# Kernel optimization log

Measured on AMD Instinct MI355X. Metric: run time of the kernel, lower is better.

The kernel has to match this reference:

```python
import jax, jax.numpy as jnp
import numpy as np

B, S, D, H, L = 32, 512, 512, 8, 6
NQ, FF, V, C = 8, 2048, 32000, 10
DK = D // H
EPS = 1e-5


def _layernorm(x, g, b):
    mu = jnp.mean(x, axis=-1, keepdims=True)
    var = jnp.mean(jnp.square(x - mu), axis=-1, keepdims=True)
    return (x - mu) * jax.lax.rsqrt(var + EPS) * g + b


def _pos_encoding(seq_len, dim):
    pos = jnp.arange(seq_len, dtype=jnp.float32)[:, None]
    div = jnp.exp(jnp.arange(0, dim, 2, dtype=jnp.float32) * (-jnp.log(10000.0) / dim))
    pe = jnp.zeros((seq_len, dim), dtype=jnp.float32)
    pe = pe.at[:, 0::2].set(jnp.sin(pos * div))
    pe = pe.at[:, 1::2].set(jnp.cos(pos * div))
    return pe


def setup_inputs() -> dict:
    key = jax.random.key(0)
    ks = jax.random.split(key, 16)
    sd = 0.02
    return {
        "x": jax.random.randint(ks[0], (B, S), 0, V),
        "emb": jax.random.normal(ks[1], (V, D), jnp.float32) * sd,
        "ln1_g": jnp.ones((L, D), jnp.float32),
        "ln1_b": jnp.zeros((L, D), jnp.float32),
        "ln2_g": jnp.ones((L, D), jnp.float32),
        "ln2_b": jnp.zeros((L, D), jnp.float32),
        "attn_w": jax.random.normal(ks[2], (L, D, D), jnp.float32) * sd,
        "attn_b": jnp.zeros((L, D), jnp.float32),
        "theta": jax.random.normal(ks[3], (L, NQ), jnp.float32),
        "ffn_w1": jax.random.normal(ks[4], (L, NQ, FF), jnp.float32) * sd,
        "ffn_b1": jnp.zeros((L, FF), jnp.float32),
        "ffn_w2": jax.random.normal(ks[5], (L, FF, D), jnp.float32) * sd,
        "ffn_b2": jnp.zeros((L, D), jnp.float32),
        "clf_w": jax.random.normal(ks[6], (D, C), jnp.float32) * sd,
        "clf_b": jnp.zeros((C,), jnp.float32),
    }


def reference(x, emb, ln1_g, ln1_b, ln2_g, ln2_b, attn_w, attn_b, theta,
              ffn_w1, ffn_b1, ffn_w2, ffn_b2, clf_w, clf_b):
    h = emb[x] + _pos_encoding(S, D)[None]  # [B,S,D]
    scale = 1.0 / jnp.sqrt(jnp.float32(DK))
    for l in range(L):
        # --- MultiHeadAttentionQuantum: q=k=v=reshape(x), no projections ---
        q = h.reshape(B, S, H, DK)
        scores = jnp.einsum('bihd,bjhd->bhij', q, q) * scale
        p = jax.nn.softmax(scores, axis=-1)
        attn = jnp.einsum('bhij,bjhd->bihd', p, q).reshape(B, S, D)
        attn = attn @ attn_w[l] + attn_b[l]
        h = _layernorm(h + attn, ln1_g[l], ln1_b[l])
        # --- FeedForwardQuantum: per-wire RX-encode -> RY(theta) -> <Z> = cos(x)cos(theta) ---
        qout = jnp.cos(h[..., :NQ]) * jnp.cos(theta[l])  # [B,S,NQ]
        f = jax.nn.relu(qout @ ffn_w1[l] + ffn_b1[l]) @ ffn_w2[l] + ffn_b2[l]
        h = _layernorm(h + f, ln2_g[l], ln2_b[l])
    pooled = jnp.mean(h, axis=1)  # [B,D]
    return pooled @ clf_w + clf_b  # [B,C]
```

## Files before the change

### kernel.cpp

```cpp
#include <hip/hip_runtime.h>
#include <hip/hip_bf16.h>
#include <math.h>

#define BB 32
#define SS 512
#define DD 512
#define HH 8
#define DK 64
#define LL 6
#define NQ 8
#define FF 2048
#define CC 10

typedef unsigned int uint;
typedef unsigned short ushort_t;
using bf16x8 = __attribute__((ext_vector_type(8))) short;
using f32x4  = __attribute__((ext_vector_type(4))) float;

#define MFMA(a, b, c) __builtin_amdgcn_mfma_f32_16x16x32_bf16((a), (b), (c), 0, 0, 0)

union U8 { ushort_t u[8]; bf16x8 v; };

__device__ inline ushort_t f2bf(float x) {
    uint u = __float_as_uint(x);
    u += 0x7FFFu + ((u >> 16) & 1u);
    return (ushort_t)(u >> 16);
}
__device__ inline void tsplit(float v, ushort_t& hi, ushort_t& lo) {
    uint u = __float_as_uint(v);
    hi = (ushort_t)(u >> 16);
    lo = f2bf(v - __uint_as_float(u & 0xFFFF0000u));
}
__device__ inline void tsplit_fast(float v, ushort_t& hi, ushort_t& lo) {
    uint u = __float_as_uint(v);
    hi = (ushort_t)(u >> 16);
    float res = v - __uint_as_float(u & 0xFFFF0000u);
    lo = (ushort_t)(__float_as_uint(res) >> 16);
}
__device__ inline uint packsplit(float v) {
    uint u = __float_as_uint(v) & 0xFFFF0000u;
    uint ru = __float_as_uint(v - __uint_as_float(u));
    ru += 0x7FFFu + ((ru >> 16) & 1u);
    return u | (ru >> 16);
}
__device__ inline float unpackf(uint u) {
    return __uint_as_float(u & 0xFFFF0000u) + __uint_as_float(u << 16);
}

__global__ __launch_bounds__(256) void embed_pe(const int* __restrict__ x,
                                                const float* __restrict__ emb,
                                                uint* __restrict__ Hp) {
    int idx = blockIdx.x * 256 + threadIdx.x;
    if (idx >= BB * SS * DD) return;
    int d = idx & (DD - 1);
    int s = (idx >> 9) & (SS - 1);
    int tok = x[idx >> 9];
    int i2 = d >> 1;
    float freq = expf((float)(2 * i2) * (-9.210340371976184f / (float)DD));
    float ang = (float)s * freq;
    float pe = (d & 1) ? cosf(ang) : sinf(ang);
    Hp[idx] = packsplit(emb[(size_t)tok * DD + d] + pe);
}

__global__ __launch_bounds__(256) void transpose_split_w(const float* __restrict__ in,
                                                         ushort_t* __restrict__ outh,
                                                         ushort_t* __restrict__ outl,
                                                         int K, int N) {
    __shared__ ushort_t th[64][68], tl[64][68];
    int nb = N >> 6;
    int k0 = ((int)blockIdx.x / nb) << 6;
    int n0 = ((int)blockIdx.x % nb) << 6;
    int t = threadIdx.x;
    int r = t >> 2, cb = (t & 3) << 4;
#pragma unroll
    for (int c = 0; c < 4; c++) {
        float4 v = *reinterpret_cast<const float4*>(&in[(size_t)(k0 + r) * N + n0 + cb + 4 * c]);
        float vv[4] = {v.x, v.y, v.z, v.w};
#pragma unroll
        for (int e = 0; e < 4; e++) {
            ushort_t hb, lb; tsplit(vv[e], hb, lb);
            th[r][cb + 4 * c + e] = hb;
            tl[r][cb + 4 * c + e] = lb;
        }
    }
    __syncthreads();
    int n = t >> 2, kb = (t & 3) << 4;
#pragma unroll
    for (int c = 0; c < 4; c++) {
        ushort4 oh, ol;
        oh.x = th[kb + 4 * c + 0][n]; ol.x = tl[kb + 4 * c + 0][n];
        oh.y = th[kb + 4 * c + 1][n]; ol.y = tl[kb + 4 * c + 1][n];
        oh.z = th[kb + 4 * c + 2][n]; ol.z = tl[kb + 4 * c + 2][n];
        oh.w = th[kb + 4 * c + 3][n]; ol.w = tl[kb + 4 * c + 3][n];
        *reinterpret_cast<ushort4*>(&outh[(size_t)(n0 + n) * K + k0 + kb + 4 * c]) = oh;
        *reinterpret_cast<ushort4*>(&outl[(size_t)(n0 + n) * K + k0 + kb + 4 * c]) = ol;
    }
}

__global__ __launch_bounds__(256) void prep_w1t(const float* __restrict__ W1all,
                                                ushort_t* __restrict__ outh,
                                                ushort_t* __restrict__ outl) {
    int l = blockIdx.y;
    int f = blockIdx.x * 256 + threadIdx.x;
    const float* W1 = W1all + (size_t)l * NQ * FF;
    U8 ph, pl;
#pragma unroll
    for (int n = 0; n < 8; n++) {
        ushort_t hb, lb; tsplit(W1[n * FF + f], hb, lb);
        ph.u[n] = hb; pl.u[n] = lb;
    }
    *reinterpret_cast<bf16x8*>(&outh[((size_t)l * FF + f) * 8]) = ph.v;
    *reinterpret_cast<bf16x8*>(&outl[((size_t)l * FF + f) * 8]) = pl.v;
}

__global__ __launch_bounds__(256, 2) void flash_attn_split(const uint* __restrict__ Hp,
                                                           ushort_t* __restrict__ outh,
                                                           ushort_t* __restrict__ outl) {
    __shared__ __align__(16) ushort_t Qh[64][72], Ql[64][72];
    __shared__ __align__(16) ushort_t Kh[64][72], Kl[64][72];
    __shared__ __align__(16) ushort_t Vh[64][72], Vl[64][72];
    __shared__ __align__(16) ushort_t Ph[64][72], Pl[64][72];

    int i0 = blockIdx.x * 64;
    int h0 = blockIdx.y * DK;
    int b  = blockIdx.z;
    const uint* baseH = Hp + (size_t)b * (SS * DD);

    int t = threadIdx.x;
    int w = t >> 6;
    int ln = t & 63;
    int l15 = ln & 15, lh = ln >> 4;

    {
        int r = t >> 2, cb = (t & 3) << 4;
        const uint* src = &baseH[(size_t)(i0 + r) * DD + h0 + cb];
#pragma unroll
        for (int g = 0; g < 2; g++) {
            U8 qh, ql;
#pragma unroll
            for (int c = 0; c < 2; c++) {
                uint4 pv = *reinterpret_cast<const uint4*>(src + g * 8 + c * 4);
                uint uu[4] = {pv.x, pv.y, pv.z, pv.w};
#pragma unroll
                for (int e = 0; e < 4; e++) {
                    qh.u[c * 4 + e] = (ushort_t)(uu[e] >> 16);
                    ql.u[c * 4 + e] = (ushort_t)(uu[e] & 0xFFFFu);
                }
            }
            *reinterpret_cast<bf16x8*>(&Qh[r][cb + g * 8]) = qh.v;
            *reinterpret_cast<bf16x8*>(&Ql[r][cb + g * 8]) = ql.v;
        }
    }

    float m_[4], l_[4], al[4];
    f32x4 acc[4];
    f32x4 z4 = {0.f, 0.f, 0.f, 0.f};
#pragma unroll
    for (int r = 0; r < 4; r++) { m_[r] = -1e30f; l_[r] = 0.f; acc[r] = z4; }

    for (int j0 = 0; j0 < SS; j0 += 64) {
        __syncthreads();
        {
            int r = t >> 2, cb = (t & 3) << 4;
            const uint* src = &baseH[(size_t)(j0 + r) * DD + h0 + cb];
#pragma unroll
            for (int g = 0; g < 2; g++) {
                U8 kh, kl;
#pragma unroll
                for (int c = 0; c < 2; c++) {
                    uint4 pv = *reinterpret_cast<const uint4*>(src + g * 8 + c * 4);
                    uint uu[4] = {pv.x, pv.y, pv.z, pv.w};
#pragma unroll
                    for (int e = 0; e < 4; e++) {
                        ushort_t hb = (ushort_t)(uu[e] >> 16);
                        ushort_t lb = (ushort_t)(uu[e] & 0xFFFFu);
                        kh.u[c * 4 + e] = hb;
                        kl.u[c * 4 + e] = lb;
                        int d = cb + g * 8 + c * 4 + e;
                        Vh[d][r] = hb;
                        Vl[d][r] = lb;
                    }
                }
                *reinterpret_cast<bf16x8*>(&Kh[r][cb + g * 8]) = kh.v;
                *reinterpret_cast<bf16x8*>(&Kl[r][cb + g * 8]) = kl.v;
            }
        }
        __syncthreads();

        f32x4 sc[4];
        bf16x8 aqh0 = *reinterpret_cast<const bf16x8*>(&Qh[w * 16 + l15][lh * 8]);
        bf16x8 aqh1 = *reinterpret_cast<const bf16x8*>(&Qh[w * 16 + l15][32 + lh * 8]);
        bf16x8 aql0 = *reinterpret_cast<const bf16x8*>(&Ql[w * 16 + l15][lh * 8]);
        bf16x8 aql1 = *reinterpret_cast<const bf16x8*>(&Ql[w * 16 + l15][32 + lh * 8]);
#pragma unroll
        for (int tt = 0; tt < 4; tt++) {
            bf16x8 bh0 = *reinterpret_cast<const bf16x8*>(&Kh[tt * 16 + l15][lh * 8]);
            bf16x8 bh1 = *reinterpret_cast<const bf16x8*>(&Kh[tt * 16 + l15][32 + lh * 8]);
            bf16x8 bl0 = *reinterpret_cast<const bf16x8*>(&Kl[tt * 16 + l15][lh * 8]);
            bf16x8 bl1 = *reinterpret_cast<const bf16x8*>(&Kl[tt * 16 + l15][32 + lh * 8]);
            f32x4 s = z4;
            s = MFMA(aqh0, bh0, s);
            s = MFMA(aqh1, bh1, s);
            s = MFMA(aqh0, bl0, s);
            s = MFMA(aqh1, bl1, s);
            s = MFMA(aql0, bh0, s);
            s = MFMA(aql1, bh1, s);
            sc[tt] = s * 0.125f;
        }

#pragma unroll
        for (int r = 0; r < 4; r++) {
            float mx = fmaxf(fmaxf(sc[0][r], sc[1][r]), fmaxf(sc[2][r], sc[3][r]));
            mx = fmaxf(mx, __shfl_xor(mx, 1));
            mx = fmaxf(mx, __shfl_xor(mx, 2));
            mx = fmaxf(mx, __shfl_xor(mx, 4));
            mx = fmaxf(mx, __shfl_xor(mx, 8));
            float nm = fmaxf(m_[r], mx);
            al[r] = __expf(m_[r] - nm);
            m_[r] = nm;
            float rs = 0.f;
#pragma unroll
            for (int tt = 0; tt < 4; tt++) {
                float p = __expf(sc[tt][r] - nm);
                sc[tt][r] = p;
                rs += p;
            }
            rs += __shfl_xor(rs, 1);
            rs += __shfl_xor(rs, 2);
            rs += __shfl_xor(rs, 4);
            rs += __shfl_xor(rs, 8);
            l_[r] = l_[r] * al[r] + rs;
        }
#pragma unroll
        for (int tt = 0; tt < 4; tt++)
#pragma unroll
            for (int r = 0; r < 4; r++) {
                ushort_t hb, lb; tsplit(sc[tt][r], hb, lb);
                Ph[w * 16 + lh * 4 + r][tt * 16 + l15] = hb;
                Pl[w * 16 + lh * 4 + r][tt * 16 + l15] = lb;
            }
#pragma unroll
        for (int td = 0; td < 4; td++) {
            acc[td][0] *= al[0];
            acc[td][1] *= al[1];
            acc[td][2] *= al[2];
            acc[td][3] *= al[3];
        }
        bf16x8 aph0 = *reinterpret_cast<const bf16x8*>(&Ph[w * 16 + l15][lh * 8]);
        bf16x8 aph1 = *reinterpret_cast<const bf16x8*>(&Ph[w * 16 + l15][32 + lh * 8]);
        bf16x8 apl0 = *reinterpret_cast<const bf16x8*>(&Pl[w * 16 + l15][lh * 8]);
        bf16x8 apl1 = *reinterpret_cast<const bf16x8*>(&Pl[w * 16 + l15][32 + lh * 8]);
#pragma unroll
        for (int td = 0; td < 4; td++) {
            bf16x8 bvh0 = *reinterpret_cast<const bf16x8*>(&Vh[td * 16 + l15][lh * 8]);
            bf16x8 bvh1 = *reinterpret_cast<const bf16x8*>(&Vh[td * 16 + l15][32 + lh * 8]);
            bf16x8 bvl0 = *reinterpret_cast<const bf16x8*>(&Vl[td * 16 + l15][lh * 8]);
            bf16x8 bvl1 = *reinterpret_cast<const bf16x8*>(&Vl[td * 16 + l15][32 + lh * 8]);
            acc[td] = MFMA(aph0, bvh0, acc[td]);
            acc[td] = MFMA(aph1, bvh1, acc[td]);
            acc[td] = MFMA(aph0, bvl0, acc[td]);
            acc[td] = MFMA(aph1, bvl1, acc[td]);
            acc[td] = MFMA(apl0, bvh0, acc[td]);
            acc[td] = MFMA(apl1, bvh1, acc[td]);
        }
    }

#pragma unroll
    for (int r = 0; r < 4; r++) {
        float inv = 1.f / l_[r];
        int row = i0 + w * 16 + lh * 4 + r;
#pragma unroll
        for (int td = 0; td < 4; td++) {
            float o = acc[td][r] * inv;
            ushort_t hb, lb; tsplit(o, hb, lb);
            size_t idx = (size_t)b * SS * DD + (size_t)row * DD + h0 + td * 16 + l15;
            outh[idx] = hb;
            outl[idx] = lb;
        }
    }
}

__global__ __launch_bounds__(256, 2) void gemm_split(const ushort_t* __restrict__ Ah,
                                                     const ushort_t* __restrict__ Al,
                                                     const ushort_t* __restrict__ Bth,
                                                     const ushort_t* __restrict__ Btl,
                                                     const float* __restrict__ bias,
                                                     float* __restrict__ C,
                                                     int M, int N, int K) {
    __shared__ __align__(16) ushort_t Abh[128][72], Abl[128][72];
    __shared__ __align__(16) ushort_t Bbh[128][72], Bbl[128][72];
    int nb = N >> 7;
    int m0 = ((int)blockIdx.x / nb) << 7;
    int n0 = ((int)blockIdx.x % nb) << 7;
    int t = threadIdx.x;
    int w = t >> 6, ln = t & 63, l15 = ln & 15, lh = ln >> 4;
    int wr = (w >> 1) * 64, wc = (w & 1) * 64;

    f32x4 z4 = {0.f, 0.f, 0.f, 0.f};
    f32x4 acc[4][4];
#pragma unroll
    for (int i = 0; i < 4; i++)
#pragma unroll
        for (int j = 0; j < 4; j++) acc[i][j] = z4;

    int arr = t >> 3, akk = (t & 7) * 8;

    for (int k0 = 0; k0 < K; k0 += 64) {
        __syncthreads();
#pragma unroll
        for (int r = 0; r < 4; r++) {
            int row = arr + r * 32;
            *reinterpret_cast<uint4*>(&Abh[row][akk]) =
                *reinterpret_cast<const uint4*>(&Ah[(size_t)(m0 + row) * K + k0 + akk]);
            *reinterpret_cast<uint4*>(&Abl[row][akk]) =
                *reinterpret_cast<const uint4*>(&Al[(size_t)(m0 + row) * K + k0 + akk]);
            *reinterpret_cast<uint4*>(&Bbh[row][akk]) =
                *reinterpret_cast<const uint4*>(&Bth[(size_t)(n0 + row) * K + k0 + akk]);
            *reinterpret_cast<uint4*>(&Bbl[row][akk]) =
                *reinterpret_cast<const uint4*>(&Btl[(size_t)(n0 + row) * K + k0 + akk]);
        }
        __syncthreads();
#pragma unroll
        for (int ks = 0; ks < 2; ks++) {
            bf16x8 ah[4], al_[4];
#pragma unroll
            for (int mt = 0; mt < 4; mt++) {
                ah[mt]  = *reinterpret_cast<const bf16x8*>(&Abh[wr + mt * 16 + l15][ks * 32 + lh * 8]);
                al_[mt] = *reinterpret_cast<const bf16x8*>(&Abl[wr + mt * 16 + l15][ks * 32 + lh * 8]);
            }
#pragma unroll
            for (int nt = 0; nt < 4; nt++) {
                bf16x8 bh = *reinterpret_cast<const bf16x8*>(&Bbh[wc + nt * 16 + l15][ks * 32 + lh * 8]);
                bf16x8 bl = *reinterpret_cast<const bf16x8*>(&Bbl[wc + nt * 16 + l15][ks * 32 + lh * 8]);
#pragma unroll
                for (int mt = 0; mt < 4; mt++) {
                    acc[mt][nt] = MFMA(ah[mt], bh, acc[mt][nt]);
                    acc[mt][nt] = MFMA(ah[mt], bl, acc[mt][nt]);
                    acc[mt][nt] = MFMA(al_[mt], bh, acc[mt][nt]);
                }
            }
        }
    }
#pragma unroll
    for (int nt = 0; nt < 4; nt++) {
        int col = n0 + wc + nt * 16 + l15;
        float bs = bias[col];
#pragma unroll
        for (int mt = 0; mt < 4; mt++)
#pragma unroll
            for (int r = 0; r < 4; r++)
                C[(size_t)(m0 + wr + mt * 16 + lh * 4 + r) * N + col] = acc[mt][nt][r] + bs;
    }
}

__global__ __launch_bounds__(256) void ln_residual(uint* __restrict__ Hp,
                                                   const float* __restrict__ add,
                                                   const float* __restrict__ g,
                                                   const float* __restrict__ bta) {
    int row = blockIdx.x * 4 + (threadIdx.x >> 6);
    int lane = threadIdx.x & 63;
    uint* hp = Hp + (size_t)row * DD;
    const float* ap = add + (size_t)row * DD;
    float v[8];
    float sum = 0.f;
#pragma unroll
    for (int i = 0; i < 8; i++) {
        int d = lane + i * 64;
        v[i] = unpackf(hp[d]) + ap[d];
        sum += v[i];
    }
#pragma unroll
    for (int off = 32; off > 0; off >>= 1) sum += __shfl_xor(sum, off);
    float mu = sum * (1.f / DD);
    float s2 = 0.f;
#pragma unroll
    for (int i = 0; i < 8; i++) {
        float d2 = v[i] - mu;
        s2 += d2 * d2;
    }
#pragma unroll
    for (int off = 32; off > 0; off >>= 1) s2 += __shfl_xor(s2, off);
    float inv = rsqrtf(s2 * (1.f / DD) + 1e-5f);
#pragma unroll
    for (int i = 0; i < 8; i++) {
        int d = lane + i * 64;
        hp[d] = packsplit((v[i] - mu) * inv * g[d] + bta[d]);
    }
}

__global__ __launch_bounds__(256, 2) void ffn_split(const uint* __restrict__ Hp,
                                                    const ushort_t* __restrict__ W1th,
                                                    const ushort_t* __restrict__ W1tl,
                                                    const float* __restrict__ b1,
                                                    const ushort_t* __restrict__ W2th,
                                                    const ushort_t* __restrict__ W2tl,
                                                    const float* __restrict__ b2,
                                                    const float* __restrict__ theta,
                                                    float* __restrict__ outp) {
    __shared__ __align__(16) ushort_t Abh[128][72], Abl[128][72];
    __shared__ __align__(16) ushort_t Bbh[128][72], Bbl[128][72];
    __shared__ __align__(16) ushort_t qsh[129][8], qsl[129][8];
    __shared__ float tcs[8];

    int t = threadIdx.x;
    int m0 = (int)(blockIdx.x >> 2) * 128;
    int n0 = (int)(blockIdx.x & 3) * 128;
    if (t < 8) {
        tcs[t] = cosf(theta[t]);
        qsh[128][t] = 0;
        qsl[128][t] = 0;
    }
    __syncthreads();
#pragma unroll
    for (int i = 0; i < 4; i++) {
        int idx = t + i * 256;
        int m = idx >> 3, n = idx & 7;
        float q = cosf(unpackf(Hp[(size_t)(m0 + m) * DD + n])) * tcs[n];
        ushort_t hb, lb; tsplit(q, hb, lb);
        qsh[m][n] = hb;
        qsl[m][n] = lb;
    }

    int w = t >> 6, ln = t & 63, l15 = ln & 15, lh = ln >> 4;
    int wr = (w >> 1) * 64, wc = (w & 1) * 64;
    bool lh0 = (lh == 0);
    f32x4 z4 = {0.f, 0.f, 0.f, 0.f};
    bf16x8 z8 = {0, 0, 0, 0, 0, 0, 0, 0};
    f32x4 acc[4][4];
#pragma unroll
    for (int i = 0; i < 4; i++)
#pragma unroll
        for (int j = 0; j < 4; j++) acc[i][j] = z4;

    int brr = t >> 3, bkk = (t & 7) * 8;

    for (int k0 = 0; k0 < FF; k0 += 64) {
        __syncthreads();
#pragma unroll
        for (int r = 0; r < 4; r++) {
            int row = brr + r * 32;
            *reinterpret_cast<uint4*>(&Bbh[row][bkk]) =
                *reinterpret_cast<const uint4*>(&W2th[(size_t)(n0 + row) * FF + k0 + bkk]);
            *reinterpret_cast<uint4*>(&Bbl[row][bkk]) =
                *reinterpret_cast<const uint4*>(&W2tl[(size_t)(n0 + row) * FF + k0 + bkk]);
        }
        bf16x8 wh[4], wl[4];
#pragma unroll
        for (int fq = 0; fq < 4; fq++) {
            bf16x8 h8 = *reinterpret_cast<const bf16x8*>(&W1th[(size_t)(k0 + fq * 16 + l15) * 8]);
            bf16x8 l8 = *reinterpret_cast<const bf16x8*>(&W1tl[(size_t)(k0 + fq * 16 + l15) * 8]);
            wh[fq] = lh0 ? h8 : z8;
            wl[fq] = lh0 ? l8 : z8;
        }
#pragma unroll
        for (int mqi = 0; mqi < 2; mqi++) {
            int m = (w * 2 + mqi) * 16 + l15;
            int mrow = lh0 ? m : 128;
            bf16x8 qh  = *reinterpret_cast<const bf16x8*>(&qsh[mrow][0]);
            bf16x8 ql_ = *reinterpret_cast<const bf16x8*>(&qsl[mrow][0]);
#pragma unroll
            for (int fq = 0; fq < 4; fq++) {
                f32x4 d = z4;
                d = MFMA(wh[fq], qh, d);
                d = MFMA(wh[fq], ql_, d);
                d = MFMA(wl[fq], qh, d);
                float4 b1v = *reinterpret_cast<const float4*>(&b1[k0 + fq * 16 + lh * 4]);
                float v0 = fmaxf(d[0] + b1v.x, 0.f);
                float v1 = fmaxf(d[1] + b1v.y, 0.f);
                float v2 = fmaxf(d[2] + b1v.z, 0.f);
                float v3 = fmaxf(d[3] + b1v.w, 0.f);
                ushort_t h0_, l0_, h1_, l1_, h2_, l2_, h3_, l3_;
                tsplit_fast(v0, h0_, l0_);
                tsplit_fast(v1, h1_, l1_);
                tsplit_fast(v2, h2_, l2_);
                tsplit_fast(v3, h3_, l3_);
                uint2 hu, lu;
                hu.x = (uint)h0_ | ((uint)h1_ << 16);
                hu.y = (uint)h2_ | ((uint)h3_ << 16);
                lu.x = (uint)l0_ | ((uint)l1_ << 16);
                lu.y = (uint)l2_ | ((uint)l3_ << 16);
                *reinterpret_cast<uint2*>(&Abh[m][fq * 16 + lh * 4]) = hu;
                *reinterpret_cast<uint2*>(&Abl[m][fq * 16 + lh * 4]) = lu;
            }
        }
        __syncthreads();
#pragma unroll
        for (int ks = 0; ks < 2; ks++) {
            bf16x8 ah[4], al_[4];
#pragma unroll
            for (int mt = 0; mt < 4; mt++) {
                ah[mt]  = *reinterpret_cast<const bf16x8*>(&Abh[wr + mt * 16 + l15][ks * 32 + lh * 8]);
                al_[mt] = *reinterpret_cast<const bf16x8*>(&Abl[wr + mt * 16 + l15][ks * 32 + lh * 8]);
            }
#pragma unroll
            for (int nt = 0; nt < 4; nt++) {
                bf16x8 bh = *reinterpret_cast<const bf16x8*>(&Bbh[wc + nt * 16 + l15][ks * 32 + lh * 8]);
                bf16x8 bl = *reinterpret_cast<const bf16x8*>(&Bbl[wc + nt * 16 + l15][ks * 32 + lh * 8]);
#pragma unroll
                for (int mt = 0; mt < 4; mt++) {
                    acc[mt][nt] = MFMA(ah[mt], bh, acc[mt][nt]);
                    acc[mt][nt] = MFMA(ah[mt], bl, acc[mt][nt]);
                    acc[mt][nt] = MFMA(al_[mt], bh, acc[mt][nt]);
                }
            }
        }
    }
#pragma unroll
    for (int nt = 0; nt < 4; nt++) {
        int col = n0 + wc + nt * 16 + l15;
        float bs = b2[col];
#pragma unroll
        for (int mt = 0; mt < 4; mt++)
#pragma unroll
            for (int r = 0; r < 4; r++)
                outp[(size_t)(m0 + wr + mt * 16 + lh * 4 + r) * DD + col] = acc[mt][nt][r] + bs;
    }
}

__global__ __launch_bounds__(256) void pool_mean(const uint* __restrict__ Hp,
                                                 float* __restrict__ pooled) {
    int idx = blockIdx.x * 256 + threadIdx.x;
    if (idx >= BB * DD) return;
    int b = idx >> 9, d = idx & 511;
    float s = 0.f;
    for (int j = 0; j < SS; j++) s += unpackf(Hp[((size_t)b * SS + j) * DD + d]);
    pooled[idx] = s * (1.f / SS);
}

__global__ __launch_bounds__(64) void classifier(const float* __restrict__ pooled,
                                                 const float* __restrict__ W,
                                                 const float* __restrict__ bias,
                                                 float* __restrict__ out) {
    int o = blockIdx.x;
    int b = o / CC, c = o % CC;
    int lane = threadIdx.x;
    float s = 0.f;
    for (int d = lane; d < DD; d += 64) s += pooled[b * DD + d] * W[d * CC + c];
#pragma unroll
    for (int off = 32; off > 0; off >>= 1) s += __shfl_xor(s, off);
    if (lane == 0) out[o] = s + bias[c];
}

extern "C" void kernel_launch(void* const* d_in, const int* in_sizes, int n_in,
                              void* d_out, int out_size, void* d_ws, size_t ws_size,
                              hipStream_t stream) {
    (void)in_sizes; (void)n_in; (void)out_size; (void)ws_size;
    const int*   x      = (const int*)d_in[0];
    const float* emb    = (const float*)d_in[1];
    const float* ln1_g  = (const float*)d_in[2];
    const float* ln1_b  = (const float*)d_in[3];
    const float* ln2_g  = (const float*)d_in[4];
    const float* ln2_b  = (const float*)d_in[5];
    const float* attn_w = (const float*)d_in[6];
    const float* attn_b = (const float*)d_in[7];
    const float* theta  = (const float*)d_in[8];
    const float* ffn_w1 = (const float*)d_in[9];
    const float* ffn_b1 = (const float*)d_in[10];
    const float* ffn_w2 = (const float*)d_in[11];
    const float* ffn_b2 = (const float*)d_in[12];
    const float* clf_w  = (const float*)d_in[13];
    const float* clf_b  = (const float*)d_in[14];
    float* out = (float*)d_out;

    char* ws = (char*)d_ws;
    uint*     Hp     = (uint*)(ws);
    float*    t2     = (float*)(ws + 33554432);
    ushort_t* t1h    = (ushort_t*)(ws + 67108864);
    ushort_t* t1l    = (ushort_t*)(ws + 83886080);
    float*    pooled = (float*)(ws + 100663296);
    ushort_t* Wath   = (ushort_t*)(ws + 100728832);
    ushort_t* Watl   = (ushort_t*)(ws + 101253120);
    ushort_t* W1th6  = (ushort_t*)(ws + 101777408);
    ushort_t* W1tl6  = (ushort_t*)(ws + 101974016);
    ushort_t* W2th   = (ushort_t*)(ws + 67108864);
    ushort_t* W2tl   = (ushort_t*)(ws + 67108864 + 2097152);

    embed_pe<<<(BB * SS * DD + 255) / 256, 256, 0, stream>>>(x, emb, Hp);
    prep_w1t<<<dim3(FF / 256, LL), 256, 0, stream>>>(ffn_w1, W1th6, W1tl6);

    for (int l = 0; l < LL; l++) {
        flash_attn_split<<<dim3(SS / 64, HH, BB), 256, 0, stream>>>(Hp, t1h, t1l);
        transpose_split_w<<<(DD / 64) * (DD / 64), 256, 0, stream>>>(
            attn_w + (size_t)l * DD * DD, Wath, Watl, DD, DD);
        gemm_split<<<(16384 / 128) * (DD / 128), 256, 0, stream>>>(
            t1h, t1l, Wath, Watl, attn_b + l * DD, t2, BB * SS, DD, DD);
        ln_residual<<<BB * SS / 4, 256, 0, stream>>>(Hp, t2, ln1_g + l * DD, ln1_b + l * DD);
        transpose_split_w<<<(FF / 64) * (DD / 64), 256, 0, stream>>>(
            ffn_w2 + (size_t)l * FF * DD, W2th, W2tl, FF, DD);
        ffn_split<<<(16384 / 128) * (DD / 128), 256, 0, stream>>>(
            Hp, W1th6 + (size_t)l * FF * 8, W1tl6 + (size_t)l * FF * 8, ffn_b1 + l * FF,
            W2th, W2tl, ffn_b2 + l * DD, theta + l * NQ, t2);
        ln_residual<<<BB * SS / 4, 256, 0, stream>>>(Hp, t2, ln2_g + l * DD, ln2_b + l * DD);
    }

    pool_mean<<<(BB * DD + 255) / 256, 256, 0, stream>>>(Hp, pooled);
    classifier<<<BB * CC, 64, 0, stream>>>(pooled, clf_w, clf_b, out);
}
```

Before: 2.022 ms.

## Enlarge attention query tile to 128 rows with 512 threads, Q in registers

Each attention block now handles 128 query rows with 8 waves instead of 64 rows with 4 waves, which halves the K/V global loads and bf16 hi/lo splitting per query row. Q fragments are loaded straight into registers rather than staged through shared memory. V is now built by transposing the K tile already in shared memory, instead of scattered element stores during the global load. The cost is an extra barrier per key tile, a larger P buffer, and tighter register limits from the 512x4 launch bounds, which could cause spills or lower occupancy.

```diff
diff --git a/kernel.cpp b/kernel.cpp
--- a/kernel.cpp
+++ b/kernel.cpp
@@ -113,15 +113,14 @@
     *reinterpret_cast<bf16x8*>(&outl[((size_t)l * FF + f) * 8]) = pl.v;
 }
 
-__global__ __launch_bounds__(256, 2) void flash_attn_split(const uint* __restrict__ Hp,
+__global__ __launch_bounds__(512, 4) void flash_attn_split(const uint* __restrict__ Hp,
                                                            ushort_t* __restrict__ outh,
                                                            ushort_t* __restrict__ outl) {
-    __shared__ __align__(16) ushort_t Qh[64][72], Ql[64][72];
     __shared__ __align__(16) ushort_t Kh[64][72], Kl[64][72];
     __shared__ __align__(16) ushort_t Vh[64][72], Vl[64][72];
-    __shared__ __align__(16) ushort_t Ph[64][72], Pl[64][72];
-
-    int i0 = blockIdx.x * 64;
+    __shared__ __align__(16) ushort_t Ph[128][72], Pl[128][72];
+
+    int i0 = blockIdx.x * 128;
     int h0 = blockIdx.y * DK;
     int b  = blockIdx.z;
     const uint* baseH = Hp + (size_t)b * (SS * DD);
@@ -131,25 +130,25 @@
     int ln = t & 63;
     int l15 = ln & 15, lh = ln >> 4;
 
+    bf16x8 aqh0, aqh1, aql0, aql1;
     {
-        int r = t >> 2, cb = (t & 3) << 4;
-        const uint* src = &baseH[(size_t)(i0 + r) * DD + h0 + cb];
-#pragma unroll
-        for (int g = 0; g < 2; g++) {
-            U8 qh, ql;
-#pragma unroll
-            for (int c = 0; c < 2; c++) {
-                uint4 pv = *reinterpret_cast<const uint4*>(src + g * 8 + c * 4);
-                uint uu[4] = {pv.x, pv.y, pv.z, pv.w};
-#pragma unroll
-                for (int e = 0; e < 4; e++) {
-                    qh.u[c * 4 + e] = (ushort_t)(uu[e] >> 16);
-                    ql.u[c * 4 + e] = (ushort_t)(uu[e] & 0xFFFFu);
-                }
-            }
-            *reinterpret_cast<bf16x8*>(&Qh[r][cb + g * 8]) = qh.v;
-            *reinterpret_cast<bf16x8*>(&Ql[r][cb + g * 8]) = ql.v;
-        }
+        int row = i0 + w * 16 + l15;
+        const uint* src = &baseH[(size_t)row * DD + h0 + lh * 8];
+        uint4 p0 = *reinterpret_cast<const uint4*>(src);
+        uint4 p1 = *reinterpret_cast<const uint4*>(src + 4);
+        uint4 p2 = *reinterpret_cast<const uint4*>(src + 32);
+        uint4 p3 = *reinterpret_cast<const uint4*>(src + 36);
+        uint a0[8] = {p0.x, p0.y, p0.z, p0.w, p1.x, p1.y, p1.z, p1.w};
+        uint a1[8] = {p2.x, p2.y, p2.z, p2.w, p3.x, p3.y, p3.z, p3.w};
+        U8 h0u, l0u, h1u, l1u;
+#pragma unroll
+        for (int e = 0; e < 8; e++) {
+            h0u.u[e] = (ushort_t)(a0[e] >> 16);
+            l0u.u[e] = (ushort_t)(a0[e] & 0xFFFFu);
+            h1u.u[e] = (ushort_t)(a1[e] >> 16);
+            l1u.u[e] = (ushort_t)(a1[e] & 0xFFFFu);
+        }
+        aqh0 = h0u.v; aql0 = l0u.v; aqh1 = h1u.v; aql1 = l1u.v;
     }
 
     float m_[4], l_[4], al[4];
@@ -158,40 +157,33 @@
 #pragma unroll
     for (int r = 0; r < 4; r++) { m_[r] = -1e30f; l_[r] = 0.f; acc[r] = z4; }
 
+    int kr = t >> 3, kcb = (t & 7) * 8;
+    int vc = t & 7, vr = t >> 3;
+
     for (int j0 = 0; j0 < SS; j0 += 64) {
         __syncthreads();
         {
-            int r = t >> 2, cb = (t & 3) << 4;
-            const uint* src = &baseH[(size_t)(j0 + r) * DD + h0 + cb];
-#pragma unroll
-            for (int g = 0; g < 2; g++) {
-                U8 kh, kl;
-#pragma unroll
-                for (int c = 0; c < 2; c++) {
-                    uint4 pv = *reinterpret_cast<const uint4*>(src + g * 8 + c * 4);
-                    uint uu[4] = {pv.x, pv.y, pv.z, pv.w};
-#pragma unroll
-                    for (int e = 0; e < 4; e++) {
-                        ushort_t hb = (ushort_t)(uu[e] >> 16);
-                        ushort_t lb = (ushort_t)(uu[e] & 0xFFFFu);
-                        kh.u[c * 4 + e] = hb;
-                        kl.u[c * 4 + e] = lb;
-                        int d = cb + g * 8 + c * 4 + e;
-                        Vh[d][r] = hb;
-                        Vl[d][r] = lb;
-                    }
-                }
-                *reinterpret_cast<bf16x8*>(&Kh[r][cb + g * 8]) = kh.v;
-                *reinterpret_cast<bf16x8*>(&Kl[r][cb + g * 8]) = kl.v;
-            }
-        }
-        __syncthreads();
-
+            const uint* src = &baseH[(size_t)(j0 + kr) * DD + h0 + kcb];
+            uint4 p0 = *reinterpret_cast<const uint4*>(src);
+            uint4 p1 = *reinterpret_cast<const uint4*>(src + 4);
+            uint a[8] = {p0.x, p0.y, p0.z, p0.w, p1.x, p1.y, p1.z, p1.w};
+            U8 kh, kl;
+#pragma unroll
+            for (int e = 0; e < 8; e++) {
+                kh.u[e] = (ushort_t)(a[e] >> 16);
+                kl.u[e] = (ushort_t)(a[e] & 0xFFFFu);
+            }
+            *reinterpret_cast<bf16x8*>(&Kh[kr][kcb]) = kh.v;
+            *reinterpret_cast<bf16x8*>(&Kl[kr][kcb]) = kl.v;
+        }
+        __syncthreads();
+#pragma unroll
+        for (int e = 0; e < 8; e++) {
+            int d = vc + 8 * e;
+            Vh[d][vr] = Kh[vr][d];
+            Vl[d][vr] = Kl[vr][d];
+        }
         f32x4 sc[4];
-        bf16x8 aqh0 = *reinterpret_cast<const bf16x8*>(&Qh[w * 16 + l15][lh * 8]);
-        bf16x8 aqh1 = *reinterpret_cast<const bf16x8*>(&Qh[w * 16 + l15][32 + lh * 8]);
-        bf16x8 aql0 = *reinterpret_cast<const bf16x8*>(&Ql[w * 16 + l15][lh * 8]);
-        bf16x8 aql1 = *reinterpret_cast<const bf16x8*>(&Ql[w * 16 + l15][32 + lh * 8]);
 #pragma unroll
         for (int tt = 0; tt < 4; tt++) {
             bf16x8 bh0 = *reinterpret_cast<const bf16x8*>(&Kh[tt * 16 + l15][lh * 8]);
@@ -207,7 +199,6 @@
             s = MFMA(aql1, bh1, s);
             sc[tt] = s * 0.125f;
         }
-
 #pragma unroll
         for (int r = 0; r < 4; r++) {
             float mx = fmaxf(fmaxf(sc[0][r], sc[1][r]), fmaxf(sc[2][r], sc[3][r]));
@@ -239,6 +230,7 @@
                 Ph[w * 16 + lh * 4 + r][tt * 16 + l15] = hb;
                 Pl[w * 16 + lh * 4 + r][tt * 16 + l15] = lb;
             }
+        __syncthreads();
 #pragma unroll
         for (int td = 0; td < 4; td++) {
             acc[td][0] *= al[0];
@@ -579,7 +571,7 @@
     prep_w1t<<<dim3(FF / 256, LL), 256, 0, stream>>>(ffn_w1, W1th6, W1tl6);
 
     for (int l = 0; l < LL; l++) {
-        flash_attn_split<<<dim3(SS / 64, HH, BB), 256, 0, stream>>>(Hp, t1h, t1l);
+        flash_attn_split<<<dim3(SS / 128, HH, BB), 512, 0, stream>>>(Hp, t1h, t1l);
         transpose_split_w<<<(DD / 64) * (DD / 64), 256, 0, stream>>>(
             attn_w + (size_t)l * DD * DD, Wath, Watl, DD, DD);
         gemm_split<<<(16384 / 128) * (DD / 128), 256, 0, stream>>>(
```

New measurement: 1.867 ms. 1.08x faster.
